# Kernel optimization log

Hardware: AMD Instinct MI355X
Metric: run time of the kernel (lower is better)

## Reference

```python
import jax, jax.numpy as jnp
import numpy as np
from jax import lax

B, T, C_IN, HW = 16, 2048, 17, 8
N_CONV, HID, OUT = 4, 150, 2
IN_SZ = N_CONV * 6 * 6  # 144


def setup_inputs() -> dict:
    key = jax.random.key(0)
    ks = jax.random.split(key, 9)
    s = lambda *sh: 1.0 / np.sqrt(sh[-1])
    return {
        "inputs": jax.random.normal(ks[0], (B, T, C_IN, HW, HW), jnp.float32),
        "conv_w": jax.random.normal(ks[1], (N_CONV, C_IN, 3, 3), jnp.float32) * 0.1,
        "conv_b": jax.random.normal(ks[2], (N_CONV,), jnp.float32) * 0.1,
        "w_ih": jax.random.normal(ks[3], (4 * HID, IN_SZ), jnp.float32) * s(IN_SZ),
        "w_hh": jax.random.normal(ks[4], (4 * HID, HID), jnp.float32) * s(HID),
        "b_ih": jax.random.normal(ks[5], (4 * HID,), jnp.float32) * s(HID),
        "b_hh": jax.random.normal(ks[6], (4 * HID,), jnp.float32) * s(HID),
        "last_w": jax.random.normal(ks[7], (OUT, HID), jnp.float32) * s(HID),
        "last_b": jax.random.normal(ks[8], (OUT,), jnp.float32) * s(HID),
    }


def reference(inputs, conv_w, conv_b, w_ih, w_hh, b_ih, b_hh, last_w, last_b):
    b, t = inputs.shape[:2]
    # Conv2d over all timesteps at once (same math as the per-step loop).
    x = inputs.reshape(b * t, C_IN, HW, HW)
    y = lax.conv_general_dilated(
        x, conv_w, window_strides=(1, 1), padding="VALID",
        dimension_numbers=("NCHW", "OIHW", "NCHW"),
    ) + conv_b[None, :, None, None]           # [B*T, 4, 6, 6]
    y = jax.nn.relu(y).reshape(b, t, IN_SZ)   # [B, T, 144]
    # Precompute input-to-gate projection for every step (batched GEMM).
    gates_x = jnp.einsum("btf,gf->btg", y, w_ih) + b_ih + b_hh  # [B, T, 600]

    def step(carry, gx):
        h, c = carry
        g = gx + h @ w_hh.T  # [B, 600]; PyTorch gate order: i, f, g, o
        i, f, gg, o = jnp.split(g, 4, axis=-1)
        c = jax.nn.sigmoid(f) * c + jax.nn.sigmoid(i) * jnp.tanh(gg)
        h = jax.nn.sigmoid(o) * jnp.tanh(c)
        return (h, c), None

    h0 = jnp.zeros((b, HID), inputs.dtype)
    (hT, _), _ = lax.scan(step, (h0, h0), jnp.swapaxes(gates_x, 0, 1))
    return hT @ last_w.T + last_b  # [B, 2] == last(h_T).squeeze()
```

## Files before the change

### kernel.cpp

```cpp
#include <hip/hip_runtime.h>

typedef _Float16 f16;
typedef _Float16 f16x4 __attribute__((ext_vector_type(4)));
typedef _Float16 f16x8 __attribute__((ext_vector_type(8)));
typedef float f32x4 __attribute__((ext_vector_type(4)));
typedef int i32x4 __attribute__((ext_vector_type(4)));

#define TLEN 2048
#define TPAD 2050
#define NCOL 640
#define GSTEP (16 * NCOL)
#define NPROD 240
#define NCHUNK 256
#define K1 1.4426950408889634f
#define K2 2.8853900817779268f

__global__ __launch_bounds__(64) void rowmax_k(const float* __restrict__ w_hh,
                                               float* __restrict__ rowmax)
{
    const int r = blockIdx.x * 64 + threadIdx.x;
    if (r < 600) {
        float m = 0.f;
        for (int k = 0; k < 150; ++k) m = fmaxf(m, fabsf(w_hh[r * 150 + k]));
        rowmax[r] = m;
    }
}

__global__ void prep_weights(const float* __restrict__ w_ih,
                             const float* __restrict__ w_hh,
                             const float* __restrict__ b_ih,
                             const float* __restrict__ b_hh,
                             const float* __restrict__ rowmax,
                             f16* __restrict__ wihf, signed char* __restrict__ whhq,
                             float* __restrict__ biasp, float* __restrict__ dsc)
{
    const int idx = blockIdx.x * blockDim.x + threadIdx.x;
    const int stride = gridDim.x * blockDim.x;
    for (int i = idx; i < 40 * 5 * 64 * 8; i += stride) {
        const int e = i & 7;
        const int lane = (i >> 3) & 63;
        const int kt = (i >> 9) % 5;
        const int nt = i / 2560;
        const int colg = nt * 16 + (lane & 15);
        const int u = colg >> 2, G = colg & 3;
        const int k = kt * 32 + (lane >> 4) * 8 + e;
        const float sc = (G == 2) ? K2 : -K1;
        f16 vi = (f16)0.f;
        if (u < 150 && k < 144) vi = (f16)(w_ih[(G * 150 + u) * 144 + k] * sc);
        wihf[i] = vi;
    }
    for (int i = idx; i < 40 * 3 * 64 * 16; i += stride) {
        const int byte = i & 15;
        const int lane = (i >> 4) & 63;
        const int kt = (i >> 10) % 3;
        const int nt = i / 3072;
        const int colg = nt * 16 + (lane & 15);
        const int u = colg >> 2, G = colg & 3;
        const int k = kt * 64 + (lane >> 4) * 16 + byte;
        signed char q = 0;
        if (u < 150 && k < 150) {
            const int row = G * 150 + u;
            const float rm = rowmax[row];
            if (rm > 0.f)
                q = (signed char)(int)rintf(w_hh[row * 150 + k] * (127.f / rm));
        }
        whhq[i] = q;
    }
    for (int i = idx; i < NCOL; i += stride) {
        const int u = i >> 2, G = i & 3;
        const float sc = (G == 2) ? K2 : -K1;
        biasp[i] = (u < 150) ? (b_ih[G * 150 + u] + b_hh[G * 150 + u]) * sc : 0.f;
        dsc[i]   = (u < 150) ? sc * rowmax[G * 150 + u] * (1.f / 16129.f) : 0.f;
    }
}

__device__ __forceinline__ void lstm_stepQ(
    int t, int cur, f16x4& pfu, f16x4& pfc, const f16*& pLoad,
    const i32x4 (&afrag)[5][3], const f32x4& scv,
    signed char* hqs, f16* hfs, float& cst,
    int grp, int sel, bool wr, int u)
{
    const f16x4 pnew = *(const f16x4*)pLoad;
    pLoad += GSTEP;

    const signed char* hr = hqs + cur * 192 + grp * 16;
    i32x4 bf[3];
    #pragma unroll
    for (int kt = 0; kt < 3; ++kt)
        bf[kt] = *(const i32x4*)(hr + kt * 64);

    float gx0 = (float)pfu[0], gx1 = (float)pfu[1];
    float gx2 = (float)pfu[2], gx3 = (float)pfu[3];
    pfc = pnew;

    const i32x4 zc = {0, 0, 0, 0};
    i32x4 acc[5];
    #pragma unroll
    for (int i = 0; i < 5; ++i)
        acc[i] = __builtin_amdgcn_mfma_i32_16x16x64_i8(afrag[i][0], bf[0], zc, 0, 0, 0);
    #pragma unroll
    for (int kt = 1; kt < 3; ++kt)
        #pragma unroll
        for (int i = 0; i < 5; ++i)
            acc[i] = __builtin_amdgcn_mfma_i32_16x16x64_i8(afrag[i][kt], bf[kt], acc[i], 0, 0, 0);

    int s0 = acc[0][0], s1 = acc[0][1], s2 = acc[0][2], s3 = acc[0][3];
    #pragma unroll
    for (int i = 1; i < 5; ++i) {
        const bool p = (sel == i);
        s0 = p ? acc[i][0] : s0;
        s1 = p ? acc[i][1] : s1;
        s2 = p ? acc[i][2] : s2;
        s3 = p ? acc[i][3] : s3;
    }

    const float g0 = fmaf((float)s0, scv[0], gx0);
    const float g1 = fmaf((float)s1, scv[1], gx1);
    const float g2 = fmaf((float)s2, scv[2], gx2);
    const float g3 = fmaf((float)s3, scv[3], gx3);

    const float ei = __builtin_amdgcn_exp2f(g0);
    const float ef = __builtin_amdgcn_exp2f(g1);
    const float eg = __builtin_amdgcn_exp2f(fminf(g2, 38.f));
    const float eo = __builtin_amdgcn_exp2f(g3);
    const float dig = (1.f + ei) * (eg + 1.f);
    const float c = cst * __builtin_amdgcn_rcpf(1.f + ef)
                  + (eg - 1.f) * __builtin_amdgcn_rcpf(dig);
    cst = c;
    const float ec = __builtin_amdgcn_exp2f(fminf(K2 * c, 80.f));
    const float h = (ec - 1.f) * __builtin_amdgcn_rcpf((1.f + eo) * (ec + 1.f));

    if (wr) hqs[(cur ^ 1) * 192 + u] = (signed char)(int)rintf(127.f * h);
    if (t == TLEN - 1 && wr) hfs[u] = (f16)h;

    asm volatile("s_waitcnt lgkmcnt(0)" ::: "memory");
    __builtin_amdgcn_s_barrier();
    __builtin_amdgcn_sched_barrier(0);
}

__global__ __launch_bounds__(512, 1) void mega(
    const float* __restrict__ inp, const float* __restrict__ cw,
    const float* __restrict__ cb,
    const f16* __restrict__ wihf, const float* __restrict__ biasp,
    f16* __restrict__ gates3,
    const signed char* __restrict__ whhq, const float* __restrict__ dsc,
    const float* __restrict__ last_w, const float* __restrict__ last_b,
    int* __restrict__ flags, float* __restrict__ out)
{
    const int bid = blockIdx.x;
    const int tid = threadIdx.x, w = tid >> 6, lane = tid & 63;
    const int col = lane & 15, grp = lane >> 4;

    if (bid >= 16) {
        __shared__ float s_in[16][1092];
        __shared__ __align__(16) f16 s_y[8][16][168];
        __shared__ float s_w[612];
        for (int i = tid; i < 612; i += 512) s_w[i] = cw[i];

        f16x8 bfr[5][5];
        float bb[5];
        #pragma unroll
        for (int i = 0; i < 5; ++i) {
            const int nt = w * 5 + i;
            const f16* wf = wihf + (size_t)(nt * 5) * 512;
            #pragma unroll
            for (int kt = 0; kt < 5; ++kt)
                bfr[i][kt] = *(const f16x8*)(wf + kt * 512 + lane * 8);
            bb[i] = biasp[nt * 16 + col];
        }
        const int cb_b = tid & 15, unit = tid >> 4;
        const int oc = unit / 6, oy = unit % 6;
        const float cbias = (unit < 24) ? cb[oc] : 0.f;
        __syncthreads();

        for (int ch = bid - 16; ch < NCHUNK; ch += NPROD) {
            const int t0 = ch * 8;
            for (int tl = 0; tl < 8; ++tl) {
                const int t = t0 + tl;
                __syncthreads();
                {
                    const int si = tid >> 5, l2 = tid & 31;
                    const float* ip = inp + ((size_t)si * TLEN + t) * 1088;
                    for (int k = l2; k < 1088; k += 32) s_in[si][k] = ip[k];
                }
                __syncthreads();
                if (unit < 24) {
                    const float* wp = s_w + oc * 153;
                    float acc[6] = {cbias, cbias, cbias, cbias, cbias, cbias};
                    #pragma unroll 1
                    for (int ic = 0; ic < 17; ++ic) {
                        const float* rowb = &s_in[cb_b][ic * 64 + oy * 8];
                        #pragma unroll
                        for (int ky = 0; ky < 3; ++ky) {
                            const float* r = rowb + ky * 8;
                            const float w0 = wp[ic * 9 + ky * 3 + 0];
                            const float w1 = wp[ic * 9 + ky * 3 + 1];
                            const float w2 = wp[ic * 9 + ky * 3 + 2];
                            #pragma unroll
                            for (int ox = 0; ox < 6; ++ox)
                                acc[ox] += r[ox] * w0 + r[ox + 1] * w1 + r[ox + 2] * w2;
                        }
                    }
                    #pragma unroll
                    for (int ox = 0; ox < 6; ++ox)
                        s_y[tl][cb_b][oc * 36 + oy * 6 + ox] = (f16)fmaxf(acc[ox], 0.f);
                } else if (unit == 24) {
                    #pragma unroll
                    for (int k = 0; k < 16; ++k) s_y[tl][cb_b][144 + k] = (f16)0.f;
                }
            }
            __syncthreads();
            for (int tl = 0; tl < 8; ++tl) {
                const int t = t0 + tl;
                f16x8 a[5];
                #pragma unroll
                for (int kt = 0; kt < 5; ++kt)
                    a[kt] = *(const f16x8*)(&s_y[tl][col][kt * 32 + grp * 8]);
                #pragma unroll
                for (int i = 0; i < 5; ++i) {
                    f32x4 acc = {0.f, 0.f, 0.f, 0.f};
                    #pragma unroll
                    for (int kt = 0; kt < 5; ++kt)
                        acc = __builtin_amdgcn_mfma_f32_16x16x32_f16(a[kt], bfr[i][kt], acc, 0, 0, 0);
                    const int colg = (w * 5 + i) * 16 + col;
                    #pragma unroll
                    for (int r = 0; r < 4; ++r)
                        gates3[((size_t)(t * 16 + grp * 4 + r)) * NCOL + colg] =
                            (f16)(acc[r] + bb[i]);
                }
            }
            __threadfence();
            __syncthreads();
            if (tid == 0)
                __hip_atomic_store(&flags[ch], 1, __ATOMIC_RELEASE,
                                   __HIP_MEMORY_SCOPE_AGENT);
        }
        return;
    }

    __shared__ __align__(16) signed char hq[2 * 192];
    __shared__ __align__(16) f16 hf[160];
    const int b = bid;
    const int sel = (col < 5) ? col : ((col < 10) ? col - 5 : ((col < 15) ? col - 10 : 0));
    const bool wr = (col < 5);
    const int u = 20 * w + 4 * sel + grp;

    for (int i = tid; i < 2 * 192; i += 512) hq[i] = 0;

    i32x4 afrag[5][3];
    #pragma unroll
    for (int i = 0; i < 5; ++i)
        #pragma unroll
        for (int kt = 0; kt < 3; ++kt)
            afrag[i][kt] =
                *(const i32x4*)(whhq + (size_t)(((5 * w + i) * 3 + kt) * 64 + lane) * 16);

    const f32x4 scv = *(const f32x4*)(dsc + 4 * u);
    float cst = 0.f;
    __syncthreads();

    while (__hip_atomic_load(&flags[0], __ATOMIC_ACQUIRE, __HIP_MEMORY_SCOPE_AGENT) == 0)
        __builtin_amdgcn_s_sleep(2);
    int pend = __hip_atomic_load(&flags[1], __ATOMIC_ACQUIRE, __HIP_MEMORY_SCOPE_AGENT);

    const f16* gbu = gates3 + (size_t)b * NCOL + 80 * w + 16 * sel + 4 * grp;
    f16x4 pA = *(const f16x4*)(gbu);
    f16x4 pB = *(const f16x4*)(gbu + (size_t)1 * GSTEP);
    const f16* pLoad = gbu + (size_t)2 * GSTEP;

    #pragma unroll 1
    for (int tb = 0; tb < TLEN; tb += 2) {
        const int tn = tb + 2;
        if ((tn & 7) == 0 && tn < TLEN) {
            const int ch = tn >> 3;
            while (pend == 0) {
                pend = __hip_atomic_load(&flags[ch], __ATOMIC_ACQUIRE,
                                         __HIP_MEMORY_SCOPE_AGENT);
                if (!pend) __builtin_amdgcn_s_sleep(2);
            }
            pend = (ch + 1 < NCHUNK)
                 ? __hip_atomic_load(&flags[ch + 1], __ATOMIC_ACQUIRE,
                                     __HIP_MEMORY_SCOPE_AGENT)
                 : 1;
        }
        lstm_stepQ(tb,     0, pA, pA, pLoad, afrag, scv, hq, hf, cst, grp, sel, wr, u);
        lstm_stepQ(tb + 1, 1, pB, pB, pLoad, afrag, scv, hq, hf, cst, grp, sel, wr, u);
    }

    if (tid < 2) {
        float s = last_b[tid];
        for (int j = 0; j < 150; ++j)
            s += (float)hf[j] * last_w[tid * 150 + j];
        out[b * 2 + tid] = s;
    }
}

extern "C" void kernel_launch(void* const* d_in, const int* in_sizes, int n_in,
                              void* d_out, int out_size, void* d_ws, size_t ws_size,
                              hipStream_t stream) {
    const float* inp    = (const float*)d_in[0];
    const float* conv_w = (const float*)d_in[1];
    const float* conv_b = (const float*)d_in[2];
    const float* w_ih   = (const float*)d_in[3];
    const float* w_hh   = (const float*)d_in[4];
    const float* b_ih   = (const float*)d_in[5];
    const float* b_hh   = (const float*)d_in[6];
    const float* last_w = (const float*)d_in[7];
    const float* last_b = (const float*)d_in[8];
    float* out = (float*)d_out;

    char* ws = (char*)d_ws;
    size_t off = 0;
    f16*   gates3 = (f16*)(ws + off);  off += (size_t)TPAD * 16 * NCOL * 2;
    f16*   wihf   = (f16*)(ws + off);  off += 204800;
    signed char* whhq = (signed char*)(ws + off); off += 122880;
    float* biasp  = (float*)(ws + off); off += 2560;
    float* dsc    = (float*)(ws + off); off += 2560;
    float* rowmax = (float*)(ws + off); off += 2560;
    int*   flags  = (int*)(ws + off);   off += (NCHUNK + 4) * 4;

    hipMemsetAsync(flags, 0, (NCHUNK + 4) * 4, stream);
    rowmax_k<<<10, 64, 0, stream>>>(w_hh, rowmax);
    prep_weights<<<120, 256, 0, stream>>>(w_ih, w_hh, b_ih, b_hh, rowmax,
                                          wihf, whhq, biasp, dsc);
    mega<<<256, 512, 0, stream>>>(inp, conv_w, conv_b, wihf, biasp, gates3,
                                  whhq, dsc, last_w, last_b, flags, out);
}
```

Before: 1.234 ms.

## Split fused producer/consumer megakernel into separate conv-GEMM and LSTM scan kernels

The single persistent kernel, where 240 blocks produced gate chunks and 16 blocks ran the recurrence while polling flags, is replaced by two sequential launches: a conv+input-GEMM kernel over 256 blocks, then a 16-block LSTM scan. This removes the flag polling, atomics and flag memset from the recurrent loop, and all 256 blocks now work on the conv stage at once. The cost is that the scan can no longer start until every gate has been computed, so the two phases no longer overlap. The shared-memory row pitch for the input tile is also changed from 1092 to 1099.

```diff
diff --git a/kernel.cpp b/kernel.cpp
--- a/kernel.cpp
+++ b/kernel.cpp
@@ -10,8 +10,7 @@
 #define TPAD 2050
 #define NCOL 640
 #define GSTEP (16 * NCOL)
-#define NPROD 240
-#define NCHUNK 256
+#define SPITCH 1099
 #define K1 1.4426950408889634f
 #define K2 2.8853900817779268f
 
@@ -74,6 +73,92 @@
     }
 }
 
+__global__ __launch_bounds__(512, 1) void conv_gemm(
+    const float* __restrict__ inp, const float* __restrict__ cw,
+    const float* __restrict__ cb,
+    const f16* __restrict__ wihf, const float* __restrict__ biasp,
+    f16* __restrict__ gates3)
+{
+    __shared__ float s_in[16][SPITCH];
+    __shared__ __align__(16) f16 s_y[8][16][168];
+    __shared__ float s_w[612];
+    const int tid = threadIdx.x, w = tid >> 6, lane = tid & 63;
+    const int col = lane & 15, grp = lane >> 4;
+    for (int i = tid; i < 612; i += 512) s_w[i] = cw[i];
+
+    f16x8 bfr[5][5];
+    float bb[5];
+    #pragma unroll
+    for (int i = 0; i < 5; ++i) {
+        const int nt = w * 5 + i;
+        const f16* wf = wihf + (size_t)(nt * 5) * 512;
+        #pragma unroll
+        for (int kt = 0; kt < 5; ++kt)
+            bfr[i][kt] = *(const f16x8*)(wf + kt * 512 + lane * 8);
+        bb[i] = biasp[nt * 16 + col];
+    }
+    const int cb_b = tid & 15, unit = tid >> 4;
+    const int oc = unit / 6, oy = unit % 6;
+    const float cbias = (unit < 24) ? cb[oc] : 0.f;
+    __syncthreads();
+
+    const int t0 = blockIdx.x * 8;
+    for (int tl = 0; tl < 8; ++tl) {
+        const int t = t0 + tl;
+        __syncthreads();
+        {
+            const int si = tid >> 5, l2 = tid & 31;
+            const float* ip = inp + ((size_t)si * TLEN + t) * 1088;
+            for (int k = l2; k < 1088; k += 32) s_in[si][k] = ip[k];
+        }
+        __syncthreads();
+        if (unit < 24) {
+            const float* wp = s_w + oc * 153;
+            float acc[6] = {cbias, cbias, cbias, cbias, cbias, cbias};
+            #pragma unroll 1
+            for (int ic = 0; ic < 17; ++ic) {
+                const float* rowb = &s_in[cb_b][ic * 64 + oy * 8];
+                #pragma unroll
+                for (int ky = 0; ky < 3; ++ky) {
+                    const float* r = rowb + ky * 8;
+                    const float w0 = wp[ic * 9 + ky * 3 + 0];
+                    const float w1 = wp[ic * 9 + ky * 3 + 1];
+                    const float w2 = wp[ic * 9 + ky * 3 + 2];
+                    #pragma unroll
+                    for (int ox = 0; ox < 6; ++ox)
+                        acc[ox] += r[ox] * w0 + r[ox + 1] * w1 + r[ox + 2] * w2;
+                }
+            }
+            #pragma unroll
+            for (int ox = 0; ox < 6; ++ox)
+                s_y[tl][cb_b][oc * 36 + oy * 6 + ox] = (f16)fmaxf(acc[ox], 0.f);
+        } else if (unit == 24) {
+            #pragma unroll
+            for (int k = 0; k < 16; ++k) s_y[tl][cb_b][144 + k] = (f16)0.f;
+        }
+    }
+    __syncthreads();
+    for (int tl = 0; tl < 8; ++tl) {
+        const int t = t0 + tl;
+        f16x8 a[5];
+        #pragma unroll
+        for (int kt = 0; kt < 5; ++kt)
+            a[kt] = *(const f16x8*)(&s_y[tl][col][kt * 32 + grp * 8]);
+        #pragma unroll
+        for (int i = 0; i < 5; ++i) {
+            f32x4 acc = {0.f, 0.f, 0.f, 0.f};
+            #pragma unroll
+            for (int kt = 0; kt < 5; ++kt)
+                acc = __builtin_amdgcn_mfma_f32_16x16x32_f16(a[kt], bfr[i][kt], acc, 0, 0, 0);
+            const int colg = (w * 5 + i) * 16 + col;
+            #pragma unroll
+            for (int r = 0; r < 4; ++r)
+                gates3[((size_t)(t * 16 + grp * 4 + r)) * NCOL + colg] =
+                    (f16)(acc[r] + bb[i]);
+        }
+    }
+}
+
 __device__ __forceinline__ void lstm_stepQ(
     int t, int cur, f16x4& pfu, f16x4& pfc, const f16*& pLoad,
     const i32x4 (&afrag)[5][3], const f32x4& scv,
@@ -138,109 +223,17 @@
     __builtin_amdgcn_sched_barrier(0);
 }
 
-__global__ __launch_bounds__(512, 1) void mega(
-    const float* __restrict__ inp, const float* __restrict__ cw,
-    const float* __restrict__ cb,
-    const f16* __restrict__ wihf, const float* __restrict__ biasp,
-    f16* __restrict__ gates3,
-    const signed char* __restrict__ whhq, const float* __restrict__ dsc,
+__global__ __launch_bounds__(512, 1) void lstm_scan(
+    const f16* __restrict__ gates3, const signed char* __restrict__ whhq,
+    const float* __restrict__ dsc,
     const float* __restrict__ last_w, const float* __restrict__ last_b,
-    int* __restrict__ flags, float* __restrict__ out)
-{
-    const int bid = blockIdx.x;
+    float* __restrict__ out)
+{
+    __shared__ __align__(16) signed char hq[2 * 192];
+    __shared__ __align__(16) f16 hf[160];
+    const int b = blockIdx.x;
     const int tid = threadIdx.x, w = tid >> 6, lane = tid & 63;
     const int col = lane & 15, grp = lane >> 4;
-
-    if (bid >= 16) {
-        __shared__ float s_in[16][1092];
-        __shared__ __align__(16) f16 s_y[8][16][168];
-        __shared__ float s_w[612];
-        for (int i = tid; i < 612; i += 512) s_w[i] = cw[i];
-
-        f16x8 bfr[5][5];
-        float bb[5];
-        #pragma unroll
-        for (int i = 0; i < 5; ++i) {
-            const int nt = w * 5 + i;
-            const f16* wf = wihf + (size_t)(nt * 5) * 512;
-            #pragma unroll
-            for (int kt = 0; kt < 5; ++kt)
-                bfr[i][kt] = *(const f16x8*)(wf + kt * 512 + lane * 8);
-            bb[i] = biasp[nt * 16 + col];
-        }
-        const int cb_b = tid & 15, unit = tid >> 4;
-        const int oc = unit / 6, oy = unit % 6;
-        const float cbias = (unit < 24) ? cb[oc] : 0.f;
-        __syncthreads();
-
-        for (int ch = bid - 16; ch < NCHUNK; ch += NPROD) {
-            const int t0 = ch * 8;
-            for (int tl = 0; tl < 8; ++tl) {
-                const int t = t0 + tl;
-                __syncthreads();
-                {
-                    const int si = tid >> 5, l2 = tid & 31;
-                    const float* ip = inp + ((size_t)si * TLEN + t) * 1088;
-                    for (int k = l2; k < 1088; k += 32) s_in[si][k] = ip[k];
-                }
-                __syncthreads();
-                if (unit < 24) {
-                    const float* wp = s_w + oc * 153;
-                    float acc[6] = {cbias, cbias, cbias, cbias, cbias, cbias};
-                    #pragma unroll 1
-                    for (int ic = 0; ic < 17; ++ic) {
-                        const float* rowb = &s_in[cb_b][ic * 64 + oy * 8];
-                        #pragma unroll
-                        for (int ky = 0; ky < 3; ++ky) {
-                            const float* r = rowb + ky * 8;
-                            const float w0 = wp[ic * 9 + ky * 3 + 0];
-                            const float w1 = wp[ic * 9 + ky * 3 + 1];
-                            const float w2 = wp[ic * 9 + ky * 3 + 2];
-                            #pragma unroll
-                            for (int ox = 0; ox < 6; ++ox)
-                                acc[ox] += r[ox] * w0 + r[ox + 1] * w1 + r[ox + 2] * w2;
-                        }
-                    }
-                    #pragma unroll
-                    for (int ox = 0; ox < 6; ++ox)
-                        s_y[tl][cb_b][oc * 36 + oy * 6 + ox] = (f16)fmaxf(acc[ox], 0.f);
-                } else if (unit == 24) {
-                    #pragma unroll
-                    for (int k = 0; k < 16; ++k) s_y[tl][cb_b][144 + k] = (f16)0.f;
-                }
-            }
-            __syncthreads();
-            for (int tl = 0; tl < 8; ++tl) {
-                const int t = t0 + tl;
-                f16x8 a[5];
-                #pragma unroll
-                for (int kt = 0; kt < 5; ++kt)
-                    a[kt] = *(const f16x8*)(&s_y[tl][col][kt * 32 + grp * 8]);
-                #pragma unroll
-                for (int i = 0; i < 5; ++i) {
-                    f32x4 acc = {0.f, 0.f, 0.f, 0.f};
-                    #pragma unroll
-                    for (int kt = 0; kt < 5; ++kt)
-                        acc = __builtin_amdgcn_mfma_f32_16x16x32_f16(a[kt], bfr[i][kt], acc, 0, 0, 0);
-                    const int colg = (w * 5 + i) * 16 + col;
-                    #pragma unroll
-                    for (int r = 0; r < 4; ++r)
-                        gates3[((size_t)(t * 16 + grp * 4 + r)) * NCOL + colg] =
-                            (f16)(acc[r] + bb[i]);
-                }
-            }
-            __threadfence();
-            __syncthreads();
-            if (tid == 0)
-                __hip_atomic_store(&flags[ch], 1, __ATOMIC_RELEASE,
-                                   __HIP_MEMORY_SCOPE_AGENT);
-        }
-        return;
-    }
-
-    __shared__ __align__(16) signed char hq[2 * 192];
-    __shared__ __align__(16) f16 hf[160];
-    const int b = bid;
     const int sel = (col < 5) ? col : ((col < 10) ? col - 5 : ((col < 15) ? col - 10 : 0));
     const bool wr = (col < 5);
     const int u = 20 * w + 4 * sel + grp;
@@ -258,10 +251,6 @@
     const f32x4 scv = *(const f32x4*)(dsc + 4 * u);
     float cst = 0.f;
     __syncthreads();
-
-    while (__hip_atomic_load(&flags[0], __ATOMIC_ACQUIRE, __HIP_MEMORY_SCOPE_AGENT) == 0)
-        __builtin_amdgcn_s_sleep(2);
-    int pend = __hip_atomic_load(&flags[1], __ATOMIC_ACQUIRE, __HIP_MEMORY_SCOPE_AGENT);
 
     const f16* gbu = gates3 + (size_t)b * NCOL + 80 * w + 16 * sel + 4 * grp;
     f16x4 pA = *(const f16x4*)(gbu);
@@ -270,19 +259,6 @@
 
     #pragma unroll 1
     for (int tb = 0; tb < TLEN; tb += 2) {
-        const int tn = tb + 2;
-        if ((tn & 7) == 0 && tn < TLEN) {
-            const int ch = tn >> 3;
-            while (pend == 0) {
-                pend = __hip_atomic_load(&flags[ch], __ATOMIC_ACQUIRE,
-                                         __HIP_MEMORY_SCOPE_AGENT);
-                if (!pend) __builtin_amdgcn_s_sleep(2);
-            }
-            pend = (ch + 1 < NCHUNK)
-                 ? __hip_atomic_load(&flags[ch + 1], __ATOMIC_ACQUIRE,
-                                     __HIP_MEMORY_SCOPE_AGENT)
-                 : 1;
-        }
         lstm_stepQ(tb,     0, pA, pA, pLoad, afrag, scv, hq, hf, cst, grp, sel, wr, u);
         lstm_stepQ(tb + 1, 1, pB, pB, pLoad, afrag, scv, hq, hf, cst, grp, sel, wr, u);
     }
@@ -317,12 +293,10 @@
     float* biasp  = (float*)(ws + off); off += 2560;
     float* dsc    = (float*)(ws + off); off += 2560;
     float* rowmax = (float*)(ws + off); off += 2560;
-    int*   flags  = (int*)(ws + off);   off += (NCHUNK + 4) * 4;
-
-    hipMemsetAsync(flags, 0, (NCHUNK + 4) * 4, stream);
+
     rowmax_k<<<10, 64, 0, stream>>>(w_hh, rowmax);
     prep_weights<<<120, 256, 0, stream>>>(w_ih, w_hh, b_ih, b_hh, rowmax,
                                           wihf, whhq, biasp, dsc);
-    mega<<<256, 512, 0, stream>>>(inp, conv_w, conv_b, wihf, biasp, gates3,
-                                  whhq, dsc, last_w, last_b, flags, out);
-}
+    conv_gemm<<<256, 512, 0, stream>>>(inp, conv_w, conv_b, wihf, biasp, gates3);
+    lstm_scan<<<16, 512, 0, stream>>>(gates3, whhq, dsc, last_w, last_b, out);
+}
```

Measured after the change: 1.004 ms. 18.6% less time.
